# Kernel optimization log

Hardware: AMD Instinct MI355X
Metric: run time of the kernel (lower is better)

The kernel has to match this reference:

```python
import jax, jax.numpy as jnp
import numpy as np

LOAD = 0.001 / np.sqrt(2.0)  # diagonal loading applied to BOTH real and imag parts (faithful to source)


def setup_inputs() -> dict:
    key = jax.random.key(0)
    k1, k2, k3 = jax.random.split(key, 3)
    N, C, T, F = 8, 8, 600, 257
    mixture = jax.random.normal(k1, (N, 2, C, T, F), dtype=jnp.float32)
    noise = jax.random.normal(k2, (N, 2, C, T, F), dtype=jnp.float32)
    steering_vector = jax.random.normal(k3, (N, 2, F, C, 1), dtype=jnp.float32)
    return {"mixture": mixture, "noise": noise, "steering_vector": steering_vector}


def reference(mixture, noise, steering_vector):
    # to complex: RI dim is axis 1
    y = mixture[:, 0] + 1j * mixture[:, 1]            # [N,C,T,F]
    v = noise[:, 0] + 1j * noise[:, 1]                # [N,C,T,F]
    d = steering_vector[:, 0] + 1j * steering_vector[:, 1]  # [N,F,C,1]
    N, C, T, F = y.shape

    # time-averaged noise spatial covariance: mean_t v v^H  -> [N,F,C,C]
    phi = jnp.einsum('nctf,ndtf->nfcd', v, jnp.conj(v)) / T

    # diagonal loading: source adds load*eye to both real and imag stacks
    phi = phi + (LOAD + 1j * LOAD) * jnp.eye(C, dtype=phi.dtype)

    phi_inv = jnp.linalg.inv(phi)                     # [N,F,C,C]

    w_nume = phi_inv @ d                              # [N,F,C,1]
    dH = jnp.conj(jnp.swapaxes(d, -1, -2))            # [N,F,1,C]
    w_deno = dH @ phi_inv @ d                         # [N,F,1,1]
    w = w_nume / w_deno                               # [N,F,C,1]  (1x1 complex inverse)

    # beamform: X[n,t,f] = sum_c conj(w[n,f,c]) * y[n,c,t,f]
    X = jnp.einsum('nfc,nctf->ntf', jnp.conj(w[..., 0]), y)

    # back to RI-stacked [N,2,1,T,F]
    out = jnp.stack([X.real, X.imag], axis=1)[:, :, None]
    return out
```

## Files before the change

kernel.cpp:

```cpp
#include <hip/hip_runtime.h>

#define NN 8
#define CC 8
#define TT 600
#define FF 257
#define NF (NN * FF)
#define LOADING 7.0710678118654746e-04f

__global__ __launch_bounds__(256) void cov_kernel(const float* __restrict__ noise,
                                                  float* __restrict__ partial,
                                                  int tc) {
    int j = blockIdx.x * 256 + threadIdx.x;
    if (j >= NF) return;
    int n = j / FF;
    int f = j - n * FF;
    int t0 = blockIdx.y * tc;
    int t1 = t0 + tc;
    if (t1 > TT) t1 = TT;

    const float* base = noise + (size_t)n * (2 * CC * TT * FF) + f;

    float diag[CC];
    float offr[28], offi[28];
#pragma unroll
    for (int c = 0; c < CC; ++c) diag[c] = 0.f;
#pragma unroll
    for (int p = 0; p < 28; ++p) { offr[p] = 0.f; offi[p] = 0.f; }

    for (int t = t0; t < t1; ++t) {
        float vr[CC], vi[CC];
#pragma unroll
        for (int c = 0; c < CC; ++c) {
            vr[c] = base[(c * TT + t) * FF];
            vi[c] = base[((CC + c) * TT + t) * FF];
        }
        int p = 0;
#pragma unroll
        for (int c = 0; c < CC; ++c) {
            diag[c] += vr[c] * vr[c] + vi[c] * vi[c];
#pragma unroll
            for (int d2 = c + 1; d2 < CC; ++d2) {
                offr[p] += vr[c] * vr[d2] + vi[c] * vi[d2];
                offi[p] += vi[c] * vr[d2] - vr[c] * vi[d2];
                ++p;
            }
        }
    }

    float* o = partial + ((size_t)blockIdx.y * NF + j) * 64;
#pragma unroll
    for (int c = 0; c < CC; ++c) o[c] = diag[c];
#pragma unroll
    for (int p = 0; p < 28; ++p) {
        o[8 + p] = offr[p];
        o[36 + p] = offi[p];
    }
}

__global__ __launch_bounds__(64) void solve_kernel(const float* __restrict__ partial,
                                                   const float* __restrict__ steer,
                                                   float* __restrict__ wc,
                                                   int ntc) {
    int j = blockIdx.x * 64 + threadIdx.x;
    if (j >= NF) return;
    int n = j / FF;
    int f = j - n * FF;

    float acc[64];
#pragma unroll
    for (int k = 0; k < 64; ++k) acc[k] = 0.f;
    for (int tci = 0; tci < ntc; ++tci) {
        const float* p = partial + ((size_t)tci * NF + j) * 64;
#pragma unroll
        for (int k = 0; k < 16; ++k) {
            float4 v = ((const float4*)p)[k];
            acc[4 * k + 0] += v.x;
            acc[4 * k + 1] += v.y;
            acc[4 * k + 2] += v.z;
            acc[4 * k + 3] += v.w;
        }
    }

    const float invT = 1.0f / (float)TT;
    float Ar[CC][CC], Ai[CC][CC];
    {
        int p = 0;
#pragma unroll
        for (int c = 0; c < CC; ++c) {
            Ar[c][c] = acc[c] * invT + LOADING;
            Ai[c][c] = LOADING;
#pragma unroll
            for (int d2 = c + 1; d2 < CC; ++d2) {
                float re = acc[8 + p] * invT, im = acc[36 + p] * invT;
                Ar[c][d2] = re;  Ai[c][d2] = im;
                Ar[d2][c] = re;  Ai[d2][c] = -im;
                ++p;
            }
        }
    }

    float dr[CC], di[CC], br[CC], bi[CC];
#pragma unroll
    for (int c = 0; c < CC; ++c) {
        dr[c] = steer[((n * 2 + 0) * FF + f) * CC + c];
        di[c] = steer[((n * 2 + 1) * FF + f) * CC + c];
        br[c] = dr[c];
        bi[c] = di[c];
    }

#pragma unroll
    for (int k = 0; k < CC; ++k) {
        float ar = Ar[k][k], ai = Ai[k][k];
        float s = 1.0f / (ar * ar + ai * ai);
        float rr = ar * s, ri = -ai * s;
#pragma unroll
        for (int jj = k + 1; jj < CC; ++jj) {
            float xr0 = Ar[k][jj], xi0 = Ai[k][jj];
            Ar[k][jj] = xr0 * rr - xi0 * ri;
            Ai[k][jj] = xr0 * ri + xi0 * rr;
        }
        {
            float xr0 = br[k], xi0 = bi[k];
            br[k] = xr0 * rr - xi0 * ri;
            bi[k] = xr0 * ri + xi0 * rr;
        }
#pragma unroll
        for (int i = k + 1; i < CC; ++i) {
            float mr = Ar[i][k], mi = Ai[i][k];
#pragma unroll
            for (int jj = k + 1; jj < CC; ++jj) {
                float kr = Ar[k][jj], ki = Ai[k][jj];
                Ar[i][jj] -= mr * kr - mi * ki;
                Ai[i][jj] -= mr * ki + mi * kr;
            }
            float bkr = br[k], bki = bi[k];
            br[i] -= mr * bkr - mi * bki;
            bi[i] -= mr * bki + mi * bkr;
        }
    }

    float xr[CC], xi[CC];
#pragma unroll
    for (int k = CC - 1; k >= 0; --k) {
        float sr = br[k], si = bi[k];
#pragma unroll
        for (int jj = k + 1; jj < CC; ++jj) {
            sr -= Ar[k][jj] * xr[jj] - Ai[k][jj] * xi[jj];
            si -= Ar[k][jj] * xi[jj] + Ai[k][jj] * xr[jj];
        }
        xr[k] = sr;
        xi[k] = si;
    }

    float der = 0.f, dei = 0.f;
#pragma unroll
    for (int c = 0; c < CC; ++c) {
        der += dr[c] * xr[c] + di[c] * xi[c];
        dei += dr[c] * xi[c] - dr[c] * 0.f - di[c] * xr[c] + 0.f;
    }
    dei = 0.f;
#pragma unroll
    for (int c = 0; c < CC; ++c) dei += dr[c] * xi[c] - di[c] * xr[c];

    float s = 1.0f / (der * der + dei * dei);
    float* o = wc + (size_t)j * 16;
#pragma unroll
    for (int c = 0; c < CC; ++c) {
        float qr = (xr[c] * der + xi[c] * dei) * s;
        float qi = (xi[c] * der - xr[c] * dei) * s;
        o[2 * c] = qr;
        o[2 * c + 1] = -qi;
    }
}

__global__ __launch_bounds__(256) void bf_kernel(const float* __restrict__ mix,
                                                 const float* __restrict__ wc,
                                                 float* __restrict__ out) {
    int idx = blockIdx.x * 256 + threadIdx.x;
    const int perN = TT * FF;
    if (idx >= NN * perN) return;
    int n = idx / perN;
    int rem = idx - n * perN;
    int t = rem / FF;
    int f = rem - t * FF;

    const float4* w4 = (const float4*)(wc + ((size_t)(n * FF + f)) * 16);
    float4 w0 = w4[0], w1 = w4[1], w2 = w4[2], w3 = w4[3];
    float wr[CC] = {w0.x, w0.z, w1.x, w1.z, w2.x, w2.z, w3.x, w3.z};
    float wi[CC] = {w0.y, w0.w, w1.y, w1.w, w2.y, w2.w, w3.y, w3.w};

    const float* base = mix + (size_t)n * (2 * CC * TT * FF) + t * FF + f;
    float Xr = 0.f, Xi = 0.f;
#pragma unroll
    for (int c = 0; c < CC; ++c) {
        float yr = base[c * TT * FF];
        float yi = base[(CC + c) * TT * FF];
        Xr += wr[c] * yr - wi[c] * yi;
        Xi += wr[c] * yi + wi[c] * yr;
    }
    out[((size_t)(n * 2 + 0) * TT + t) * FF + f] = Xr;
    out[((size_t)(n * 2 + 1) * TT + t) * FF + f] = Xi;
}

extern "C" void kernel_launch(void* const* d_in, const int* in_sizes, int n_in,
                              void* d_out, int out_size, void* d_ws, size_t ws_size,
                              hipStream_t stream) {
    const float* mixture = (const float*)d_in[0];
    const float* noise = (const float*)d_in[1];
    const float* steer = (const float*)d_in[2];
    float* out = (float*)d_out;

    float* partial = (float*)d_ws;
    size_t per_chunk = (size_t)NF * 64 * sizeof(float);
    size_t wc_bytes = (size_t)NF * 16 * sizeof(float);
    int ntc = 25;
    while (ntc > 1 && per_chunk * (size_t)ntc + wc_bytes > ws_size) --ntc;
    int tc = (TT + ntc - 1) / ntc;
    float* wcp = partial + (size_t)ntc * NF * 64;

    dim3 gcov((NF + 255) / 256, ntc);
    cov_kernel<<<gcov, 256, 0, stream>>>(noise, partial, tc);
    solve_kernel<<<(NF + 63) / 64, 64, 0, stream>>>(partial, steer, wcp, ntc);
    int total = NN * TT * FF;
    bf_kernel<<<(total + 255) / 256, 256, 0, stream>>>(mixture, wcp, out);
}
```

Baseline: 220.0 us.

## Split covariance time chunks across waves with LDS reduction; parallelize partial summation

The covariance kernel now gives each 256-thread block 64 frequency bins and splits that block's time chunk across its four waves. The per-wave 64-value accumulators are reduced through shared memory before a single vectorized store, which gives four times more blocks and more latency hiding on the strided noise reads. The solve kernel sums the partial chunks with 64 threads per bin (one per accumulator entry), which makes those reads coalesced. A single thread then runs the 8x8 complex solve. The costs are extra shared memory and barriers in the covariance kernel, and only one active lane per wave during the solve.

```diff
diff --git a/kernel.cpp b/kernel.cpp
--- a/kernel.cpp
+++ b/kernel.cpp
@@ -4,28 +4,30 @@
 #define CC 8
 #define TT 600
 #define FF 257
-#define NF (NN * FF)
+#define NF 2056
 #define LOADING 7.0710678118654746e-04f
 
-__global__ __launch_bounds__(256) void cov_kernel(const float* __restrict__ noise,
-                                                  float* __restrict__ partial,
-                                                  int tc) {
-    int j = blockIdx.x * 256 + threadIdx.x;
-    if (j >= NF) return;
-    int n = j / FF;
-    int f = j - n * FF;
-    int t0 = blockIdx.y * tc;
-    int t1 = t0 + tc;
-    if (t1 > TT) t1 = TT;
+__global__ __launch_bounds__(256) void cov2_kernel(const float* __restrict__ noise,
+                                                   float* __restrict__ partial,
+                                                   int tc) {
+    __shared__ float red[64][128];
+    int lane = threadIdx.x & 63;
+    int wave = threadIdx.x >> 6;
+    int j = blockIdx.x * 64 + lane;
+    int jc = j < NF ? j : NF - 1;
+    int n = jc / FF;
+    int f = jc - n * FF;
+
+    int cend = min((int)(blockIdx.y + 1) * tc, TT);
+    int tsub = (tc + 3) >> 2;
+    int t0 = blockIdx.y * tc + wave * tsub;
+    int t1 = min(t0 + tsub, cend);
 
     const float* base = noise + (size_t)n * (2 * CC * TT * FF) + f;
 
-    float diag[CC];
-    float offr[28], offi[28];
-#pragma unroll
-    for (int c = 0; c < CC; ++c) diag[c] = 0.f;
-#pragma unroll
-    for (int p = 0; p < 28; ++p) { offr[p] = 0.f; offi[p] = 0.f; }
+    float acc[64];
+#pragma unroll
+    for (int k = 0; k < 64; ++k) acc[k] = 0.f;
 
     for (int t = t0; t < t1; ++t) {
         float vr[CC], vi[CC];
@@ -37,49 +39,59 @@
         int p = 0;
 #pragma unroll
         for (int c = 0; c < CC; ++c) {
-            diag[c] += vr[c] * vr[c] + vi[c] * vi[c];
+            acc[c] += vr[c] * vr[c] + vi[c] * vi[c];
 #pragma unroll
             for (int d2 = c + 1; d2 < CC; ++d2) {
-                offr[p] += vr[c] * vr[d2] + vi[c] * vi[d2];
-                offi[p] += vi[c] * vr[d2] - vr[c] * vi[d2];
+                acc[8 + p] += vr[c] * vr[d2] + vi[c] * vi[d2];
+                acc[36 + p] += vi[c] * vr[d2] - vr[c] * vi[d2];
                 ++p;
             }
         }
     }
 
-    float* o = partial + ((size_t)blockIdx.y * NF + j) * 64;
-#pragma unroll
-    for (int c = 0; c < CC; ++c) o[c] = diag[c];
-#pragma unroll
-    for (int p = 0; p < 28; ++p) {
-        o[8 + p] = offr[p];
-        o[36 + p] = offi[p];
-    }
-}
-
-__global__ __launch_bounds__(64) void solve_kernel(const float* __restrict__ partial,
-                                                   const float* __restrict__ steer,
-                                                   float* __restrict__ wc,
-                                                   int ntc) {
-    int j = blockIdx.x * 64 + threadIdx.x;
-    if (j >= NF) return;
+    if (wave >= 2) {
+        int col = threadIdx.x - 128;
+#pragma unroll
+        for (int k = 0; k < 64; ++k) red[k][col] = acc[k];
+    }
+    __syncthreads();
+    if (wave < 2) {
+#pragma unroll
+        for (int k = 0; k < 64; ++k) acc[k] += red[k][threadIdx.x];
+    }
+    __syncthreads();
+    if (wave == 1) {
+#pragma unroll
+        for (int k = 0; k < 64; ++k) red[k][lane] = acc[k];
+    }
+    __syncthreads();
+    if (wave == 0 && j < NF) {
+#pragma unroll
+        for (int k = 0; k < 64; ++k) acc[k] += red[k][lane];
+        float4* o = (float4*)(partial + ((size_t)blockIdx.y * NF + j) * 64);
+#pragma unroll
+        for (int k = 0; k < 16; ++k)
+            o[k] = make_float4(acc[4 * k], acc[4 * k + 1], acc[4 * k + 2], acc[4 * k + 3]);
+    }
+}
+
+__global__ __launch_bounds__(256) void solve2_kernel(const float* __restrict__ partial,
+                                                     const float* __restrict__ steer,
+                                                     float* __restrict__ wc,
+                                                     int ntc) {
+    __shared__ float sphi[4][64];
+    int k = threadIdx.x & 63;
+    int jj = threadIdx.x >> 6;
+    int j = blockIdx.x * 4 + jj;
+
+    float s = 0.f;
+    for (int c = 0; c < ntc; ++c) s += partial[((size_t)c * NF + j) * 64 + k];
+    sphi[jj][k] = s;
+    __syncthreads();
+
+    if (k != 0) return;
     int n = j / FF;
     int f = j - n * FF;
-
-    float acc[64];
-#pragma unroll
-    for (int k = 0; k < 64; ++k) acc[k] = 0.f;
-    for (int tci = 0; tci < ntc; ++tci) {
-        const float* p = partial + ((size_t)tci * NF + j) * 64;
-#pragma unroll
-        for (int k = 0; k < 16; ++k) {
-            float4 v = ((const float4*)p)[k];
-            acc[4 * k + 0] += v.x;
-            acc[4 * k + 1] += v.y;
-            acc[4 * k + 2] += v.z;
-            acc[4 * k + 3] += v.w;
-        }
-    }
 
     const float invT = 1.0f / (float)TT;
     float Ar[CC][CC], Ai[CC][CC];
@@ -87,11 +99,11 @@
         int p = 0;
 #pragma unroll
         for (int c = 0; c < CC; ++c) {
-            Ar[c][c] = acc[c] * invT + LOADING;
+            Ar[c][c] = sphi[jj][c] * invT + LOADING;
             Ai[c][c] = LOADING;
 #pragma unroll
             for (int d2 = c + 1; d2 < CC; ++d2) {
-                float re = acc[8 + p] * invT, im = acc[36 + p] * invT;
+                float re = sphi[jj][8 + p] * invT, im = sphi[jj][36 + p] * invT;
                 Ar[c][d2] = re;  Ai[c][d2] = im;
                 Ar[d2][c] = re;  Ai[d2][c] = -im;
                 ++p;
@@ -109,31 +121,31 @@
     }
 
 #pragma unroll
-    for (int k = 0; k < CC; ++k) {
-        float ar = Ar[k][k], ai = Ai[k][k];
-        float s = 1.0f / (ar * ar + ai * ai);
-        float rr = ar * s, ri = -ai * s;
-#pragma unroll
-        for (int jj = k + 1; jj < CC; ++jj) {
-            float xr0 = Ar[k][jj], xi0 = Ai[k][jj];
-            Ar[k][jj] = xr0 * rr - xi0 * ri;
-            Ai[k][jj] = xr0 * ri + xi0 * rr;
+    for (int kk = 0; kk < CC; ++kk) {
+        float ar = Ar[kk][kk], ai = Ai[kk][kk];
+        float sc = 1.0f / (ar * ar + ai * ai);
+        float rr = ar * sc, ri = -ai * sc;
+#pragma unroll
+        for (int c = kk + 1; c < CC; ++c) {
+            float xr0 = Ar[kk][c], xi0 = Ai[kk][c];
+            Ar[kk][c] = xr0 * rr - xi0 * ri;
+            Ai[kk][c] = xr0 * ri + xi0 * rr;
         }
         {
-            float xr0 = br[k], xi0 = bi[k];
-            br[k] = xr0 * rr - xi0 * ri;
-            bi[k] = xr0 * ri + xi0 * rr;
-        }
-#pragma unroll
-        for (int i = k + 1; i < CC; ++i) {
-            float mr = Ar[i][k], mi = Ai[i][k];
-#pragma unroll
-            for (int jj = k + 1; jj < CC; ++jj) {
-                float kr = Ar[k][jj], ki = Ai[k][jj];
-                Ar[i][jj] -= mr * kr - mi * ki;
-                Ai[i][jj] -= mr * ki + mi * kr;
+            float xr0 = br[kk], xi0 = bi[kk];
+            br[kk] = xr0 * rr - xi0 * ri;
+            bi[kk] = xr0 * ri + xi0 * rr;
+        }
+#pragma unroll
+        for (int i = kk + 1; i < CC; ++i) {
+            float mr = Ar[i][kk], mi = Ai[i][kk];
+#pragma unroll
+            for (int c = kk + 1; c < CC; ++c) {
+                float kr = Ar[kk][c], ki = Ai[kk][c];
+                Ar[i][c] -= mr * kr - mi * ki;
+                Ai[i][c] -= mr * ki + mi * kr;
             }
-            float bkr = br[k], bki = bi[k];
+            float bkr = br[kk], bki = bi[kk];
             br[i] -= mr * bkr - mi * bki;
             bi[i] -= mr * bki + mi * bkr;
         }
@@ -141,33 +153,29 @@
 
     float xr[CC], xi[CC];
 #pragma unroll
-    for (int k = CC - 1; k >= 0; --k) {
-        float sr = br[k], si = bi[k];
-#pragma unroll
-        for (int jj = k + 1; jj < CC; ++jj) {
-            sr -= Ar[k][jj] * xr[jj] - Ai[k][jj] * xi[jj];
-            si -= Ar[k][jj] * xi[jj] + Ai[k][jj] * xr[jj];
-        }
-        xr[k] = sr;
-        xi[k] = si;
+    for (int kk = CC - 1; kk >= 0; --kk) {
+        float sr = br[kk], si = bi[kk];
+#pragma unroll
+        for (int c = kk + 1; c < CC; ++c) {
+            sr -= Ar[kk][c] * xr[c] - Ai[kk][c] * xi[c];
+            si -= Ar[kk][c] * xi[c] + Ai[kk][c] * xr[c];
+        }
+        xr[kk] = sr;
+        xi[kk] = si;
     }
 
     float der = 0.f, dei = 0.f;
 #pragma unroll
     for (int c = 0; c < CC; ++c) {
         der += dr[c] * xr[c] + di[c] * xi[c];
-        dei += dr[c] * xi[c] - dr[c] * 0.f - di[c] * xr[c] + 0.f;
-    }
-    dei = 0.f;
-#pragma unroll
-    for (int c = 0; c < CC; ++c) dei += dr[c] * xi[c] - di[c] * xr[c];
-
-    float s = 1.0f / (der * der + dei * dei);
+        dei += dr[c] * xi[c] - di[c] * xr[c];
+    }
+    float sc2 = 1.0f / (der * der + dei * dei);
     float* o = wc + (size_t)j * 16;
 #pragma unroll
     for (int c = 0; c < CC; ++c) {
-        float qr = (xr[c] * der + xi[c] * dei) * s;
-        float qi = (xi[c] * der - xr[c] * dei) * s;
+        float qr = (xr[c] * der + xi[c] * dei) * sc2;
+        float qi = (xi[c] * der - xr[c] * dei) * sc2;
         o[2 * c] = qr;
         o[2 * c + 1] = -qi;
     }
@@ -218,9 +226,9 @@
     int tc = (TT + ntc - 1) / ntc;
     float* wcp = partial + (size_t)ntc * NF * 64;
 
-    dim3 gcov((NF + 255) / 256, ntc);
-    cov_kernel<<<gcov, 256, 0, stream>>>(noise, partial, tc);
-    solve_kernel<<<(NF + 63) / 64, 64, 0, stream>>>(partial, steer, wcp, ntc);
+    dim3 gcov((NF + 63) / 64, ntc);
+    cov2_kernel<<<gcov, 256, 0, stream>>>(noise, partial, tc);
+    solve2_kernel<<<NF / 4, 256, 0, stream>>>(partial, steer, wcp, ntc);
     int total = NN * TT * FF;
     bf_kernel<<<(total + 255) / 256, 256, 0, stream>>>(mixture, wcp, out);
 }
```

Measured after the change: 211.6 us. -3.8%, faster.
